# Kernel tuning notes

Hardware: AMD Instinct MI355X
Metric: run time of the kernel (lower is better)

The kernel has to match this reference:

```python
import jax, jax.numpy as jnp
import numpy as np

T = 10
CH, H, W = 16, 16, 264  # torch grid_sample sees view(1,16,16,264) as N,C,H,W
L, C = 256, 264


def _warp(img, pose):
    """Replicates F.affine_grid + F.grid_sample (bilinear, zeros padding,
    align_corners=False) on img of shape (CH,H,W) with pose=(dx,dy,dyaw)."""
    dx, dy, yaw = pose[0], pose[1], pose[2]
    cos, sin = jnp.cos(yaw), jnp.sin(yaw)
    # normalized base grid, align_corners=False: (2i+1)/N - 1
    xs = (2.0 * jnp.arange(W, dtype=img.dtype) + 1.0) / W - 1.0  # (W,)
    ys = (2.0 * jnp.arange(H, dtype=img.dtype) + 1.0) / H - 1.0  # (H,)
    gx = cos * xs[None, :] + sin * ys[:, None] + dx   # (H,W)
    gy = -sin * xs[None, :] + cos * ys[:, None] + dy  # (H,W)
    # unnormalize (align_corners=False)
    ix = ((gx + 1.0) * W - 1.0) * 0.5
    iy = ((gy + 1.0) * H - 1.0) * 0.5
    ix0 = jnp.floor(ix); iy0 = jnp.floor(iy)
    ix1 = ix0 + 1.0;     iy1 = iy0 + 1.0
    wx1 = ix - ix0; wx0 = 1.0 - wx1
    wy1 = iy - iy0; wy0 = 1.0 - wy1

    def gather(xf, yf):
        inb = (xf >= 0) & (xf < W) & (yf >= 0) & (yf < H)
        xi = jnp.clip(xf.astype(jnp.int32), 0, W - 1)
        yi = jnp.clip(yf.astype(jnp.int32), 0, H - 1)
        v = img[:, yi, xi]                      # (CH,H,W)
        return v * inb.astype(img.dtype)        # zero padding

    out = (gather(ix0, iy0) * (wx0 * wy0)
           + gather(ix1, iy0) * (wx1 * wy0)
           + gather(ix0, iy1) * (wx0 * wy1)
           + gather(ix1, iy1) * (wx1 * wy1))
    return out  # (CH,H,W)


def _forward(fuse_feature, delta_ego_pos):
    ff = fuse_feature                              # (10,256,264)
    dp = delta_ego_pos                             # (10,3)
    ff_sp = ff.reshape(T, CH, H, W)
    # prefix sums: P[k] = sum(dp[0:k]); cumulative pose for (b,t) = -sum(dp[t-1:b])
    P = jnp.concatenate([jnp.zeros((1, 3), dp.dtype), jnp.cumsum(dp, axis=0)], axis=0)
    bs = jnp.repeat(jnp.arange(T), T - 1)          # (90,) frame index
    ts = jnp.tile(jnp.arange(1, T), T)             # (90,) past-frame offset t in [1,9]
    poses = -(P[bs] - P[ts - 1])                   # (90,3)
    valid = (ts <= bs)                             # n_valid_past(b) = b
    src = ff_sp[ts]                                # (90,CH,H,W)
    warped = jax.vmap(_warp)(src, poses)           # (90,CH,H,W)
    warped = warped * valid[:, None, None, None].astype(ff.dtype)
    aligned = jnp.zeros((T, T, CH, H, W), ff.dtype)
    aligned = aligned.at[bs, (T - 1) - ts].set(warped)
    aligned = aligned.at[:, T - 1].set(ff_sp)      # current frame, unwarped
    # (B,T,L*C) self-attention fusion
    tb = aligned.reshape(T, T, L * C)
    scores = jnp.einsum('btd,bsd->bts', tb, tb)
    attn = jax.nn.softmax(scores, axis=-1)
    fused = jnp.einsum('bts,bsd->btd', attn, tb)
    fused = fused.mean(axis=1)                     # (B, L*C)
    return fused.reshape(T, L, C)                  # (10,256,264)


def setup_inputs() -> dict:
    key = jax.random.key(0)
    k1, k2 = jax.random.split(key)
    # scale features so the d=67584 dot products don't saturate the softmax
    fuse_feature = jax.random.normal(k1, (T, L, C), dtype=jnp.float32) * 0.02
    delta_ego_pos = jax.random.normal(k2, (T, 3), dtype=jnp.float32) * 0.1
    return {"fuse_feature": fuse_feature, "delta_ego_pos": delta_ego_pos}


def reference(fuse_feature, delta_ego_pos):
    return _forward(fuse_feature, delta_ego_pos)
```

## Files before the change

kernel.cpp:

```cpp
#include <hip/hip_runtime.h>
#include <math.h>

#define TT 10
#define CHN 16
#define HH 16
#define WW 264
#define HW (HH*WW)
#define DD (CHN*HW)
#define NCH 66
#define NACC 55
#define WBUF_FRAMES 45
#define WBUF_OFF 4096


__device__ __forceinline__ void pose_setup(const float* __restrict__ dp, int b,
                                           float4* __restrict__ pose) {
    if (threadIdx.x < TT-1) {
        int ts = (int)threadIdx.x + 1;
        float ax = 0.f, ay = 0.f, az = 0.f;
        for (int j = 0; j < ts-1; ++j) { ax += dp[3*j]; ay += dp[3*j+1]; az += dp[3*j+2]; }
        float bx = 0.f, by = 0.f, bz = 0.f;
        for (int j = 0; j < b; ++j)    { bx += dp[3*j]; by += dp[3*j+1]; bz += dp[3*j+2]; }
        float yaw = az - bz;
        pose[threadIdx.x] = make_float4(ax - bx, ay - by,
                                        (float)cos((double)yaw), (float)sin((double)yaw));
    }
}

__device__ __forceinline__ void plan_slot(float xs, float ys, float4 m,
                                          int& o00, int& o10, int& o01, int& o11,
                                          float& w00, float& w10, float& w01, float& w11) {
    float gx =  m.z*xs + m.w*ys + m.x;
    float gy = -m.w*xs + m.z*ys + m.y;
    float ix = ((gx + 1.f)*(float)WW - 1.f)*0.5f;
    float iy = ((gy + 1.f)*(float)HH - 1.f)*0.5f;
    float ix0f = floorf(ix), iy0f = floorf(iy);
    float wx1 = ix - ix0f, wx0 = 1.f - wx1;
    float wy1 = iy - iy0f, wy0 = 1.f - wy1;
    int ix0 = (int)ix0f, iy0 = (int)iy0f;
    int ix1 = ix0 + 1,   iy1 = iy0 + 1;
    bool inx0 = (ix0 >= 0) && (ix0 < WW);
    bool inx1 = (ix1 >= 0) && (ix1 < WW);
    bool iny0 = (iy0 >= 0) && (iy0 < HH);
    bool iny1 = (iy1 >= 0) && (iy1 < HH);
    int xi0 = min(max(ix0, 0), WW-1), xi1 = min(max(ix1, 0), WW-1);
    int yi0 = min(max(iy0, 0), HH-1), yi1 = min(max(iy1, 0), HH-1);
    float wx0m = inx0 ? wx0 : 0.f, wx1m = inx1 ? wx1 : 0.f;
    float wy0m = iny0 ? wy0 : 0.f, wy1m = iny1 ? wy1 : 0.f;
    o00 = yi0*WW + xi0; o10 = yi0*WW + xi1;
    o01 = yi1*WW + xi0; o11 = yi1*WW + xi1;
    w00 = wx0m*wy0m; w10 = wx1m*wy0m;
    w01 = wx0m*wy1m; w11 = wx1m*wy1m;
}

__device__ __forceinline__ int tri_idx(int a0, int a1) {
    return a0*TT - a0*(a0-1)/2 + (a1 - a0);
}

template<int STORE>
__global__ __launch_bounds__(256) void gram_kernel(const float* __restrict__ ff,
                                                   const float* __restrict__ dp,
                                                   float* __restrict__ scores,
                                                   float* __restrict__ wbuf) {
    int b = blockIdx.y;
    int lane = threadIdx.x & 63, wv = threadIdx.x >> 6;
    int p = blockIdx.x*64 + lane;
    __shared__ float4 pose[TT-1];
    pose_setup(dp, b, pose);
    __syncthreads();

    int y = p / WW, x = p - y*WW;
    float xs = (2.f*(float)x + 1.f)*(1.f/(float)WW) - 1.f;
    float ys = (2.f*(float)y + 1.f)*(1.f/(float)HH) - 1.f;

    float v[TT][4];
    #pragma unroll
    for (int s = 0; s < TT; ++s) {
        #pragma unroll
        for (int c = 0; c < 4; ++c) v[s][c] = 0.f;
        if (s == TT-1) {
            const float* src = ff + b*DD + (wv*4)*HW + p;
            #pragma unroll
            for (int c = 0; c < 4; ++c) v[s][c] = src[c*HW];
            continue;
        }
        int ts = (TT-1) - s;
        if (ts > b) continue;
        int o00,o10,o01,o11; float w00,w10,w01,w11;
        plan_slot(xs, ys, pose[ts-1], o00,o10,o01,o11, w00,w10,w01,w11);
        const float* src = ff + ts*DD + (wv*4)*HW;
        #pragma unroll
        for (int c = 0; c < 4; ++c) {
            const float* fc = src + c*HW;
            v[s][c] = fc[o00]*w00 + fc[o10]*w10 + fc[o01]*w01 + fc[o11]*w11;
        }
        if (STORE) {
            float* wdst = wbuf + (size_t)(b*(b-1)/2 + (ts-1))*DD + (wv*4)*HW + p;
            #pragma unroll
            for (int c = 0; c < 4; ++c) wdst[c*HW] = v[s][c];
        }
    }

    float acc[NACC];
    #pragma unroll
    for (int k = 0; k < NACC; ++k) acc[k] = 0.f;
    #pragma unroll
    for (int c = 0; c < 4; ++c) {
        int k = 0;
        #pragma unroll
        for (int t = 0; t < TT; ++t)
            #pragma unroll
            for (int s2 = t; s2 < TT; ++s2)
                acc[k++] += v[t][c]*v[s2][c];
    }

    __shared__ float red[NACC*4];
    #pragma unroll
    for (int k = 0; k < NACC; ++k) {
        float a = acc[k];
        #pragma unroll
        for (int o = 32; o > 0; o >>= 1) a += __shfl_down(a, o);
        if (lane == 0) red[k*4 + wv] = a;
    }
    __syncthreads();
    if (threadIdx.x < NACC) {
        float a = red[threadIdx.x*4] + red[threadIdx.x*4+1]
                + red[threadIdx.x*4+2] + red[threadIdx.x*4+3];
        atomicAdd(&scores[b*NACC + threadIdx.x], a);
    }
}

__device__ __forceinline__ void weights_from_scores(const float* __restrict__ scores,
                                                    int b, float* sc, float* mx_l,
                                                    float* den_l, float* wl) {
    if (threadIdx.x < NACC) sc[threadIdx.x] = scores[b*NACC + threadIdx.x];
    __syncthreads();
    if (threadIdx.x < TT) {
        int t = threadIdx.x;
        float mx = -1e30f;
        #pragma unroll
        for (int s = 0; s < TT; ++s) {
            int a0 = min(t, s), a1 = max(t, s);
            mx = fmaxf(mx, sc[tri_idx(a0, a1)]);
        }
        float den = 0.f;
        #pragma unroll
        for (int s = 0; s < TT; ++s) {
            int a0 = min(t, s), a1 = max(t, s);
            den += expf(sc[tri_idx(a0, a1)] - mx);
        }
        mx_l[t] = mx; den_l[t] = den;
    }
    __syncthreads();
    if (threadIdx.x < TT) {
        int s = threadIdx.x;
        float a2 = 0.f;
        #pragma unroll
        for (int t = 0; t < TT; ++t) {
            int a0 = min(t, s), a1 = max(t, s);
            a2 += expf(sc[tri_idx(a0, a1)] - mx_l[t]) / den_l[t];
        }
        wl[s] = a2 * 0.1f;
    }
    __syncthreads();
}

__global__ __launch_bounds__(256) void out_stream_kernel(const float* __restrict__ ff,
                                                         const float* __restrict__ scores,
                                                         const float* __restrict__ wbuf,
                                                         float* __restrict__ out) {
    int b = blockIdx.y;
    int lane = threadIdx.x & 63, wv = threadIdx.x >> 6;
    int p = blockIdx.x*64 + lane;
    __shared__ float sc[NACC];
    __shared__ float mx_l[TT], den_l[TT];
    __shared__ float wl[TT];
    weights_from_scores(scores, b, sc, mx_l, den_l, wl);

    float o[4];
    const float* idsrc = ff + b*DD + (wv*4)*HW + p;
    float wid = wl[TT-1];
    #pragma unroll
    for (int c = 0; c < 4; ++c) o[c] = wid * idsrc[c*HW];

    for (int ts = 1; ts <= b; ++ts) {
        float wb = wl[(TT-1) - ts];
        const float* src = wbuf + (size_t)(b*(b-1)/2 + (ts-1))*DD + (wv*4)*HW + p;
        #pragma unroll
        for (int c = 0; c < 4; ++c) o[c] += wb * src[c*HW];
    }
    #pragma unroll
    for (int c = 0; c < 4; ++c)
        out[(size_t)b*DD + (wv*4 + c)*HW + p] = o[c];
}

__global__ __launch_bounds__(256) void out_kernel(const float* __restrict__ ff,
                                                  const float* __restrict__ dp,
                                                  const float* __restrict__ scores,
                                                  float* __restrict__ out) {
    int b = blockIdx.y;
    int lane = threadIdx.x & 63, wv = threadIdx.x >> 6;
    int p = blockIdx.x*64 + lane;
    __shared__ float4 pose[TT-1];
    __shared__ float sc[NACC];
    __shared__ float mx_l[TT], den_l[TT];
    __shared__ float wl[TT];
    pose_setup(dp, b, pose);
    weights_from_scores(scores, b, sc, mx_l, den_l, wl);

    int y = p / WW, x = p - y*WW;
    float xs = (2.f*(float)x + 1.f)*(1.f/(float)WW) - 1.f;
    float ys = (2.f*(float)y + 1.f)*(1.f/(float)HH) - 1.f;

    float o[4] = {0.f, 0.f, 0.f, 0.f};
    #pragma unroll
    for (int s = 0; s < TT; ++s) {
        if (s == TT-1) {
            float wb = wl[s];
            const float* src = ff + b*DD + (wv*4)*HW + p;
            #pragma unroll
            for (int c = 0; c < 4; ++c) o[c] += wb*src[c*HW];
            continue;
        }
        int ts = (TT-1) - s;
        if (ts > b) continue;
        int o00,o10,o01,o11; float w00,w10,w01,w11;
        plan_slot(xs, ys, pose[ts-1], o00,o10,o01,o11, w00,w10,w01,w11);
        float wb = wl[s];
        w00 *= wb; w10 *= wb; w01 *= wb; w11 *= wb;
        const float* src = ff + ts*DD + (wv*4)*HW;
        #pragma unroll
        for (int c = 0; c < 4; ++c) {
            const float* fc = src + c*HW;
            o[c] += fc[o00]*w00 + fc[o10]*w10 + fc[o01]*w01 + fc[o11]*w11;
        }
    }
    #pragma unroll
    for (int c = 0; c < 4; ++c)
        out[(size_t)b*DD + (wv*4 + c)*HW + p] = o[c];
}

extern "C" void kernel_launch(void* const* d_in, const int* in_sizes, int n_in,
                              void* d_out, int out_size, void* d_ws, size_t ws_size,
                              hipStream_t stream) {
    const float* ff = (const float*)d_in[0];
    const float* dp = (const float*)d_in[1];
    float* out = (float*)d_out;

    float* scores = (float*)d_ws;
    float* wbuf = (float*)((char*)d_ws + WBUF_OFF);
    const size_t need = (size_t)WBUF_OFF + (size_t)WBUF_FRAMES * DD * sizeof(float);

    if (ws_size >= need) {
        gram_kernel<1><<<dim3(NCH, TT), 256, 0, stream>>>(ff, dp, scores, wbuf);
        out_stream_kernel<<<dim3(NCH, TT), 256, 0, stream>>>(ff, scores, wbuf, out);
    } else {
        gram_kernel<0><<<dim3(NCH, TT), 256, 0, stream>>>(ff, dp, scores, wbuf);
        out_kernel <<<dim3(NCH, TT), 256, 0, stream>>>(ff, dp, scores, out);
    }
}
```

Baseline: 84.82 us.

## Fuse gram and output passes into one cooperative kernel with grid sync

Replaces the two-kernel scheme, where the first pass wrote warped frames to a workspace buffer and the second re-read them, with a single cooperative kernel. Each thread keeps its warped values in registers across a grid-wide sync, then applies the softmax weights directly. This removes the workspace write and re-read traffic plus one launch, at the cost of a grid barrier and higher register pressure from the launch-bounds occupancy hint. It falls back to the two-kernel recompute path if the cooperative launch fails.

```diff
diff --git a/kernel.cpp b/kernel.cpp
--- a/kernel.cpp
+++ b/kernel.cpp
@@ -1,5 +1,8 @@
 #include <hip/hip_runtime.h>
+#include <hip/hip_cooperative_groups.h>
 #include <math.h>
+
+namespace cg = cooperative_groups;
 
 #define TT 10
 #define CHN 16
@@ -9,8 +12,6 @@
 #define DD (CHN*HW)
 #define NCH 66
 #define NACC 55
-#define WBUF_FRAMES 45
-#define WBUF_OFF 4096
 
 
 __device__ __forceinline__ void pose_setup(const float* __restrict__ dp, int b,
@@ -57,11 +58,126 @@
     return a0*TT - a0*(a0-1)/2 + (a1 - a0);
 }
 
-template<int STORE>
+__global__ __launch_bounds__(256, 3) void fused_kernel(const float* __restrict__ ff,
+                                                       const float* __restrict__ dp,
+                                                       float* __restrict__ scores,
+                                                       float* __restrict__ out) {
+    int b = blockIdx.y;
+    int lane = threadIdx.x & 63, wv = threadIdx.x >> 6;
+    int p = blockIdx.x*64 + lane;
+    __shared__ float4 pose[TT-1];
+    __shared__ float red[NACC*4];
+    __shared__ float sc[NACC];
+    __shared__ float mx_l[TT], den_l[TT];
+    __shared__ float wl[TT];
+    pose_setup(dp, b, pose);
+    __syncthreads();
+
+    int y = p / WW, x = p - y*WW;
+    float xs = (2.f*(float)x + 1.f)*(1.f/(float)WW) - 1.f;
+    float ys = (2.f*(float)y + 1.f)*(1.f/(float)HH) - 1.f;
+
+    float v[TT][4];
+    #pragma unroll
+    for (int s = 0; s < TT; ++s) {
+        #pragma unroll
+        for (int c = 0; c < 4; ++c) v[s][c] = 0.f;
+        if (s == TT-1) {
+            const float* src = ff + b*DD + (wv*4)*HW + p;
+            #pragma unroll
+            for (int c = 0; c < 4; ++c) v[s][c] = src[c*HW];
+            continue;
+        }
+        int ts = (TT-1) - s;
+        if (ts > b) continue;
+        int o00,o10,o01,o11; float w00,w10,w01,w11;
+        plan_slot(xs, ys, pose[ts-1], o00,o10,o01,o11, w00,w10,w01,w11);
+        const float* src = ff + ts*DD + (wv*4)*HW;
+        #pragma unroll
+        for (int c = 0; c < 4; ++c) {
+            const float* fc = src + c*HW;
+            v[s][c] = fc[o00]*w00 + fc[o10]*w10 + fc[o01]*w01 + fc[o11]*w11;
+        }
+    }
+
+    {
+        float acc[NACC];
+        #pragma unroll
+        for (int k = 0; k < NACC; ++k) acc[k] = 0.f;
+        #pragma unroll
+        for (int c = 0; c < 4; ++c) {
+            int k = 0;
+            #pragma unroll
+            for (int t = 0; t < TT; ++t)
+                #pragma unroll
+                for (int s2 = t; s2 < TT; ++s2)
+                    acc[k++] += v[t][c]*v[s2][c];
+        }
+        #pragma unroll
+        for (int k = 0; k < NACC; ++k) {
+            float a = acc[k];
+            #pragma unroll
+            for (int o = 32; o > 0; o >>= 1) a += __shfl_down(a, o);
+            if (lane == 0) red[k*4 + wv] = a;
+        }
+    }
+    __syncthreads();
+    if (threadIdx.x < NACC) {
+        float a = red[threadIdx.x*4] + red[threadIdx.x*4+1]
+                + red[threadIdx.x*4+2] + red[threadIdx.x*4+3];
+        atomicAdd(&scores[b*NACC + threadIdx.x], a);
+    }
+
+    cg::this_grid().sync();
+
+    if (threadIdx.x < NACC)
+        sc[threadIdx.x] = __hip_atomic_load(&scores[b*NACC + threadIdx.x],
+                                            __ATOMIC_RELAXED, __HIP_MEMORY_SCOPE_AGENT);
+    __syncthreads();
+    if (threadIdx.x < TT) {
+        int t = threadIdx.x;
+        float mx = -1e30f;
+        #pragma unroll
+        for (int s = 0; s < TT; ++s) {
+            int a0 = min(t, s), a1 = max(t, s);
+            mx = fmaxf(mx, sc[tri_idx(a0, a1)]);
+        }
+        float den = 0.f;
+        #pragma unroll
+        for (int s = 0; s < TT; ++s) {
+            int a0 = min(t, s), a1 = max(t, s);
+            den += expf(sc[tri_idx(a0, a1)] - mx);
+        }
+        mx_l[t] = mx; den_l[t] = den;
+    }
+    __syncthreads();
+    if (threadIdx.x < TT) {
+        int s = threadIdx.x;
+        float a2 = 0.f;
+        #pragma unroll
+        for (int t = 0; t < TT; ++t) {
+            int a0 = min(t, s), a1 = max(t, s);
+            a2 += expf(sc[tri_idx(a0, a1)] - mx_l[t]) / den_l[t];
+        }
+        wl[s] = a2 * 0.1f;
+    }
+    __syncthreads();
+
+    float o[4] = {0.f, 0.f, 0.f, 0.f};
+    #pragma unroll
+    for (int s = 0; s < TT; ++s) {
+        float wb = wl[s];
+        #pragma unroll
+        for (int c = 0; c < 4; ++c) o[c] += wb * v[s][c];
+    }
+    #pragma unroll
+    for (int c = 0; c < 4; ++c)
+        out[(size_t)b*DD + (wv*4 + c)*HW + p] = o[c];
+}
+
 __global__ __launch_bounds__(256) void gram_kernel(const float* __restrict__ ff,
                                                    const float* __restrict__ dp,
-                                                   float* __restrict__ scores,
-                                                   float* __restrict__ wbuf) {
+                                                   float* __restrict__ scores) {
     int b = blockIdx.y;
     int lane = threadIdx.x & 63, wv = threadIdx.x >> 6;
     int p = blockIdx.x*64 + lane;
@@ -94,11 +210,6 @@
             const float* fc = src + c*HW;
             v[s][c] = fc[o00]*w00 + fc[o10]*w10 + fc[o01]*w01 + fc[o11]*w11;
         }
-        if (STORE) {
-            float* wdst = wbuf + (size_t)(b*(b-1)/2 + (ts-1))*DD + (wv*4)*HW + p;
-            #pragma unroll
-            for (int c = 0; c < 4; ++c) wdst[c*HW] = v[s][c];
-        }
     }
 
     float acc[NACC];
@@ -128,70 +239,6 @@
                 + red[threadIdx.x*4+2] + red[threadIdx.x*4+3];
         atomicAdd(&scores[b*NACC + threadIdx.x], a);
     }
-}
-
-__device__ __forceinline__ void weights_from_scores(const float* __restrict__ scores,
-                                                    int b, float* sc, float* mx_l,
-                                                    float* den_l, float* wl) {
-    if (threadIdx.x < NACC) sc[threadIdx.x] = scores[b*NACC + threadIdx.x];
-    __syncthreads();
-    if (threadIdx.x < TT) {
-        int t = threadIdx.x;
-        float mx = -1e30f;
-        #pragma unroll
-        for (int s = 0; s < TT; ++s) {
-            int a0 = min(t, s), a1 = max(t, s);
-            mx = fmaxf(mx, sc[tri_idx(a0, a1)]);
-        }
-        float den = 0.f;
-        #pragma unroll
-        for (int s = 0; s < TT; ++s) {
-            int a0 = min(t, s), a1 = max(t, s);
-            den += expf(sc[tri_idx(a0, a1)] - mx);
-        }
-        mx_l[t] = mx; den_l[t] = den;
-    }
-    __syncthreads();
-    if (threadIdx.x < TT) {
-        int s = threadIdx.x;
-        float a2 = 0.f;
-        #pragma unroll
-        for (int t = 0; t < TT; ++t) {
-            int a0 = min(t, s), a1 = max(t, s);
-            a2 += expf(sc[tri_idx(a0, a1)] - mx_l[t]) / den_l[t];
-        }
-        wl[s] = a2 * 0.1f;
-    }
-    __syncthreads();
-}
-
-__global__ __launch_bounds__(256) void out_stream_kernel(const float* __restrict__ ff,
-                                                         const float* __restrict__ scores,
-                                                         const float* __restrict__ wbuf,
-                                                         float* __restrict__ out) {
-    int b = blockIdx.y;
-    int lane = threadIdx.x & 63, wv = threadIdx.x >> 6;
-    int p = blockIdx.x*64 + lane;
-    __shared__ float sc[NACC];
-    __shared__ float mx_l[TT], den_l[TT];
-    __shared__ float wl[TT];
-    weights_from_scores(scores, b, sc, mx_l, den_l, wl);
-
-    float o[4];
-    const float* idsrc = ff + b*DD + (wv*4)*HW + p;
-    float wid = wl[TT-1];
-    #pragma unroll
-    for (int c = 0; c < 4; ++c) o[c] = wid * idsrc[c*HW];
-
-    for (int ts = 1; ts <= b; ++ts) {
-        float wb = wl[(TT-1) - ts];
-        const float* src = wbuf + (size_t)(b*(b-1)/2 + (ts-1))*DD + (wv*4)*HW + p;
-        #pragma unroll
-        for (int c = 0; c < 4; ++c) o[c] += wb * src[c*HW];
-    }
-    #pragma unroll
-    for (int c = 0; c < 4; ++c)
-        out[(size_t)b*DD + (wv*4 + c)*HW + p] = o[c];
 }
 
 __global__ __launch_bounds__(256) void out_kernel(const float* __restrict__ ff,
@@ -206,7 +253,37 @@
     __shared__ float mx_l[TT], den_l[TT];
     __shared__ float wl[TT];
     pose_setup(dp, b, pose);
-    weights_from_scores(scores, b, sc, mx_l, den_l, wl);
+    if (threadIdx.x >= 64 && threadIdx.x < 64 + NACC)
+        sc[threadIdx.x - 64] = scores[b*NACC + (threadIdx.x - 64)];
+    __syncthreads();
+    if (threadIdx.x < TT) {
+        int t = threadIdx.x;
+        float mx = -1e30f;
+        #pragma unroll
+        for (int s = 0; s < TT; ++s) {
+            int a0 = min(t, s), a1 = max(t, s);
+            mx = fmaxf(mx, sc[tri_idx(a0, a1)]);
+        }
+        float den = 0.f;
+        #pragma unroll
+        for (int s = 0; s < TT; ++s) {
+            int a0 = min(t, s), a1 = max(t, s);
+            den += expf(sc[tri_idx(a0, a1)] - mx);
+        }
+        mx_l[t] = mx; den_l[t] = den;
+    }
+    __syncthreads();
+    if (threadIdx.x < TT) {
+        int s = threadIdx.x;
+        float a2 = 0.f;
+        #pragma unroll
+        for (int t = 0; t < TT; ++t) {
+            int a0 = min(t, s), a1 = max(t, s);
+            a2 += expf(sc[tri_idx(a0, a1)] - mx_l[t]) / den_l[t];
+        }
+        wl[s] = a2 * 0.1f;
+    }
+    __syncthreads();
 
     int y = p / WW, x = p - y*WW;
     float xs = (2.f*(float)x + 1.f)*(1.f/(float)WW) - 1.f;
@@ -246,16 +323,14 @@
     const float* ff = (const float*)d_in[0];
     const float* dp = (const float*)d_in[1];
     float* out = (float*)d_out;
-
     float* scores = (float*)d_ws;
-    float* wbuf = (float*)((char*)d_ws + WBUF_OFF);
-    const size_t need = (size_t)WBUF_OFF + (size_t)WBUF_FRAMES * DD * sizeof(float);
-
-    if (ws_size >= need) {
-        gram_kernel<1><<<dim3(NCH, TT), 256, 0, stream>>>(ff, dp, scores, wbuf);
-        out_stream_kernel<<<dim3(NCH, TT), 256, 0, stream>>>(ff, scores, wbuf, out);
-    } else {
-        gram_kernel<0><<<dim3(NCH, TT), 256, 0, stream>>>(ff, dp, scores, wbuf);
+
+    void* args[] = { (void*)&ff, (void*)&dp, (void*)&scores, (void*)&out };
+    hipError_t err = hipLaunchCooperativeKernel((void*)fused_kernel,
+                                                dim3(NCH, TT), dim3(256),
+                                                args, 0, stream);
+    if (err != hipSuccess) {
+        gram_kernel<<<dim3(NCH, TT), 256, 0, stream>>>(ff, dp, scores);
         out_kernel <<<dim3(NCH, TT), 256, 0, stream>>>(ff, dp, scores, out);
     }
 }
```

New measurement: 132.0 us. 1.56x slower.

## Drop warped-frame buffer, recompute warps and split channels across twice the blocks

Applied to the files above, without the earlier changes.

Removes the workspace path that stored warped frames in the gram kernel and streamed them back in the output kernel. The output kernel now always recomputes the bilinear warps from the input features. Each block now handles 8 channels (2 per wave) instead of 16, which doubles the grid to 1320 blocks and halves per-thread registers. This trades extra gather work in the second kernel for dropping roughly 45 frames of global writes and reads, while also raising parallelism.

```diff
diff --git a/kernel.cpp b/kernel.cpp
--- a/kernel.cpp
+++ b/kernel.cpp
@@ -9,8 +9,6 @@
 #define DD (CHN*HW)
 #define NCH 66
 #define NACC 55
-#define WBUF_FRAMES 45
-#define WBUF_OFF 4096
 
 
 __device__ __forceinline__ void pose_setup(const float* __restrict__ dp, int b,
@@ -57,14 +55,14 @@
     return a0*TT - a0*(a0-1)/2 + (a1 - a0);
 }
 
-template<int STORE>
 __global__ __launch_bounds__(256) void gram_kernel(const float* __restrict__ ff,
                                                    const float* __restrict__ dp,
-                                                   float* __restrict__ scores,
-                                                   float* __restrict__ wbuf) {
+                                                   float* __restrict__ scores) {
     int b = blockIdx.y;
+    int chunk = blockIdx.x >> 1, cgrp = blockIdx.x & 1;
     int lane = threadIdx.x & 63, wv = threadIdx.x >> 6;
-    int p = blockIdx.x*64 + lane;
+    int ch0 = cgrp*8 + wv*2;
+    int p = chunk*64 + lane;
     __shared__ float4 pose[TT-1];
     pose_setup(dp, b, pose);
     __syncthreads();
@@ -73,39 +71,34 @@
     float xs = (2.f*(float)x + 1.f)*(1.f/(float)WW) - 1.f;
     float ys = (2.f*(float)y + 1.f)*(1.f/(float)HH) - 1.f;
 
-    float v[TT][4];
+    float v[TT][2];
     #pragma unroll
     for (int s = 0; s < TT; ++s) {
         #pragma unroll
-        for (int c = 0; c < 4; ++c) v[s][c] = 0.f;
+        for (int c = 0; c < 2; ++c) v[s][c] = 0.f;
         if (s == TT-1) {
-            const float* src = ff + b*DD + (wv*4)*HW + p;
+            const float* src = ff + b*DD + ch0*HW + p;
             #pragma unroll
-            for (int c = 0; c < 4; ++c) v[s][c] = src[c*HW];
+            for (int c = 0; c < 2; ++c) v[s][c] = src[c*HW];
             continue;
         }
         int ts = (TT-1) - s;
         if (ts > b) continue;
         int o00,o10,o01,o11; float w00,w10,w01,w11;
         plan_slot(xs, ys, pose[ts-1], o00,o10,o01,o11, w00,w10,w01,w11);
-        const float* src = ff + ts*DD + (wv*4)*HW;
-        #pragma unroll
-        for (int c = 0; c < 4; ++c) {
+        const float* src = ff + ts*DD + ch0*HW;
+        #pragma unroll
+        for (int c = 0; c < 2; ++c) {
             const float* fc = src + c*HW;
             v[s][c] = fc[o00]*w00 + fc[o10]*w10 + fc[o01]*w01 + fc[o11]*w11;
         }
-        if (STORE) {
-            float* wdst = wbuf + (size_t)(b*(b-1)/2 + (ts-1))*DD + (wv*4)*HW + p;
-            #pragma unroll
-            for (int c = 0; c < 4; ++c) wdst[c*HW] = v[s][c];
-        }
     }
 
     float acc[NACC];
     #pragma unroll
     for (int k = 0; k < NACC; ++k) acc[k] = 0.f;
     #pragma unroll
-    for (int c = 0; c < 4; ++c) {
+    for (int c = 0; c < 2; ++c) {
         int k = 0;
         #pragma unroll
         for (int t = 0; t < TT; ++t)
@@ -128,70 +121,6 @@
                 + red[threadIdx.x*4+2] + red[threadIdx.x*4+3];
         atomicAdd(&scores[b*NACC + threadIdx.x], a);
     }
-}
-
-__device__ __forceinline__ void weights_from_scores(const float* __restrict__ scores,
-                                                    int b, float* sc, float* mx_l,
-                                                    float* den_l, float* wl) {
-    if (threadIdx.x < NACC) sc[threadIdx.x] = scores[b*NACC + threadIdx.x];
-    __syncthreads();
-    if (threadIdx.x < TT) {
-        int t = threadIdx.x;
-        float mx = -1e30f;
-        #pragma unroll
-        for (int s = 0; s < TT; ++s) {
-            int a0 = min(t, s), a1 = max(t, s);
-            mx = fmaxf(mx, sc[tri_idx(a0, a1)]);
-        }
-        float den = 0.f;
-        #pragma unroll
-        for (int s = 0; s < TT; ++s) {
-            int a0 = min(t, s), a1 = max(t, s);
-            den += expf(sc[tri_idx(a0, a1)] - mx);
-        }
-        mx_l[t] = mx; den_l[t] = den;
-    }
-    __syncthreads();
-    if (threadIdx.x < TT) {
-        int s = threadIdx.x;
-        float a2 = 0.f;
-        #pragma unroll
-        for (int t = 0; t < TT; ++t) {
-            int a0 = min(t, s), a1 = max(t, s);
-            a2 += expf(sc[tri_idx(a0, a1)] - mx_l[t]) / den_l[t];
-        }
-        wl[s] = a2 * 0.1f;
-    }
-    __syncthreads();
-}
-
-__global__ __launch_bounds__(256) void out_stream_kernel(const float* __restrict__ ff,
-                                                         const float* __restrict__ scores,
-                                                         const float* __restrict__ wbuf,
-                                                         float* __restrict__ out) {
-    int b = blockIdx.y;
-    int lane = threadIdx.x & 63, wv = threadIdx.x >> 6;
-    int p = blockIdx.x*64 + lane;
-    __shared__ float sc[NACC];
-    __shared__ float mx_l[TT], den_l[TT];
-    __shared__ float wl[TT];
-    weights_from_scores(scores, b, sc, mx_l, den_l, wl);
-
-    float o[4];
-    const float* idsrc = ff + b*DD + (wv*4)*HW + p;
-    float wid = wl[TT-1];
-    #pragma unroll
-    for (int c = 0; c < 4; ++c) o[c] = wid * idsrc[c*HW];
-
-    for (int ts = 1; ts <= b; ++ts) {
-        float wb = wl[(TT-1) - ts];
-        const float* src = wbuf + (size_t)(b*(b-1)/2 + (ts-1))*DD + (wv*4)*HW + p;
-        #pragma unroll
-        for (int c = 0; c < 4; ++c) o[c] += wb * src[c*HW];
-    }
-    #pragma unroll
-    for (int c = 0; c < 4; ++c)
-        out[(size_t)b*DD + (wv*4 + c)*HW + p] = o[c];
 }
 
 __global__ __launch_bounds__(256) void out_kernel(const float* __restrict__ ff,
@@ -199,27 +128,59 @@
                                                   const float* __restrict__ scores,
                                                   float* __restrict__ out) {
     int b = blockIdx.y;
+    int chunk = blockIdx.x >> 1, cgrp = blockIdx.x & 1;
     int lane = threadIdx.x & 63, wv = threadIdx.x >> 6;
-    int p = blockIdx.x*64 + lane;
+    int ch0 = cgrp*8 + wv*2;
+    int p = chunk*64 + lane;
     __shared__ float4 pose[TT-1];
     __shared__ float sc[NACC];
     __shared__ float mx_l[TT], den_l[TT];
     __shared__ float wl[TT];
     pose_setup(dp, b, pose);
-    weights_from_scores(scores, b, sc, mx_l, den_l, wl);
+    if (threadIdx.x >= 64 && threadIdx.x < 64 + NACC)
+        sc[threadIdx.x - 64] = scores[b*NACC + (threadIdx.x - 64)];
+    __syncthreads();
+    if (threadIdx.x < TT) {
+        int t = threadIdx.x;
+        float mx = -1e30f;
+        #pragma unroll
+        for (int s = 0; s < TT; ++s) {
+            int a0 = min(t, s), a1 = max(t, s);
+            mx = fmaxf(mx, sc[tri_idx(a0, a1)]);
+        }
+        float den = 0.f;
+        #pragma unroll
+        for (int s = 0; s < TT; ++s) {
+            int a0 = min(t, s), a1 = max(t, s);
+            den += expf(sc[tri_idx(a0, a1)] - mx);
+        }
+        mx_l[t] = mx; den_l[t] = den;
+    }
+    __syncthreads();
+    if (threadIdx.x < TT) {
+        int s = threadIdx.x;
+        float a2 = 0.f;
+        #pragma unroll
+        for (int t = 0; t < TT; ++t) {
+            int a0 = min(t, s), a1 = max(t, s);
+            a2 += expf(sc[tri_idx(a0, a1)] - mx_l[t]) / den_l[t];
+        }
+        wl[s] = a2 * 0.1f;
+    }
+    __syncthreads();
 
     int y = p / WW, x = p - y*WW;
     float xs = (2.f*(float)x + 1.f)*(1.f/(float)WW) - 1.f;
     float ys = (2.f*(float)y + 1.f)*(1.f/(float)HH) - 1.f;
 
-    float o[4] = {0.f, 0.f, 0.f, 0.f};
+    float o[2] = {0.f, 0.f};
     #pragma unroll
     for (int s = 0; s < TT; ++s) {
         if (s == TT-1) {
             float wb = wl[s];
-            const float* src = ff + b*DD + (wv*4)*HW + p;
+            const float* src = ff + b*DD + ch0*HW + p;
             #pragma unroll
-            for (int c = 0; c < 4; ++c) o[c] += wb*src[c*HW];
+            for (int c = 0; c < 2; ++c) o[c] += wb*src[c*HW];
             continue;
         }
         int ts = (TT-1) - s;
@@ -228,16 +189,16 @@
         plan_slot(xs, ys, pose[ts-1], o00,o10,o01,o11, w00,w10,w01,w11);
         float wb = wl[s];
         w00 *= wb; w10 *= wb; w01 *= wb; w11 *= wb;
-        const float* src = ff + ts*DD + (wv*4)*HW;
-        #pragma unroll
-        for (int c = 0; c < 4; ++c) {
+        const float* src = ff + ts*DD + ch0*HW;
+        #pragma unroll
+        for (int c = 0; c < 2; ++c) {
             const float* fc = src + c*HW;
             o[c] += fc[o00]*w00 + fc[o10]*w10 + fc[o01]*w01 + fc[o11]*w11;
         }
     }
     #pragma unroll
-    for (int c = 0; c < 4; ++c)
-        out[(size_t)b*DD + (wv*4 + c)*HW + p] = o[c];
+    for (int c = 0; c < 2; ++c)
+        out[(size_t)b*DD + (ch0 + c)*HW + p] = o[c];
 }
 
 extern "C" void kernel_launch(void* const* d_in, const int* in_sizes, int n_in,
@@ -248,14 +209,7 @@
     float* out = (float*)d_out;
 
     float* scores = (float*)d_ws;
-    float* wbuf = (float*)((char*)d_ws + WBUF_OFF);
-    const size_t need = (size_t)WBUF_OFF + (size_t)WBUF_FRAMES * DD * sizeof(float);
-
-    if (ws_size >= need) {
-        gram_kernel<1><<<dim3(NCH, TT), 256, 0, stream>>>(ff, dp, scores, wbuf);
-        out_stream_kernel<<<dim3(NCH, TT), 256, 0, stream>>>(ff, scores, wbuf, out);
-    } else {
-        gram_kernel<0><<<dim3(NCH, TT), 256, 0, stream>>>(ff, dp, scores, wbuf);
-        out_kernel <<<dim3(NCH, TT), 256, 0, stream>>>(ff, dp, scores, out);
-    }
-}
+
+    gram_kernel<<<dim3(NCH*2, TT), 256, 0, stream>>>(ff, dp, scores);
+    out_kernel <<<dim3(NCH*2, TT), 256, 0, stream>>>(ff, dp, scores, out);
+}
```

Result: slower. 103.9 us (+22.4%).
